# Kernel optimization log

Hardware: AMD Instinct MI355X
Metric: run time of the kernel (lower is better)

The kernel has to match this reference:

```python
import jax, jax.numpy as jnp
import numpy as np

B, F, H, K, E = 512, 1280, 2560, 8, 9  # batch, feat_dim, 2*feat_dim, branching, n_internal
# Tree: root=node 0 (expert 0); level-1 nodes 1..8 (experts 1..8); level-2 leaves 9..72.

def setup_inputs() -> dict:
    key = jax.random.key(0)
    k0, k1, k2, k3, k4 = jax.random.split(key, 5)
    x = jax.random.normal(k0, (B, F), dtype=jnp.float32)
    W1 = jax.random.normal(k1, (E, F, H), dtype=jnp.float32) / np.sqrt(F)
    b1 = jnp.zeros((E, H), dtype=jnp.float32)
    W2 = jax.random.normal(k2, (E, H, K), dtype=jnp.float32) / np.sqrt(H)
    b2 = jnp.zeros((E, K), dtype=jnp.float32)
    return {"x": x, "W1": W1, "b1": b1, "W2": W2, "b2": b2}

def reference(x, W1, b1, W2, b2):
    # Batched experts: Linear(F->H) -> ReLU -> Linear(H->K), softmax over children.
    h = jax.nn.relu(jnp.einsum('bf,efh->ebh', x, W1) + b1[:, None, :])  # [E,B,H]
    logits = jnp.einsum('ebh,ehk->ebk', h, W2) + b2[:, None, :]          # [E,B,K]
    probs = jax.nn.softmax(logits, axis=-1)                              # [E,B,K]
    # Path products root->node for every node (matches leaf_probs in torch code).
    p0 = jnp.ones((1, x.shape[0]), dtype=x.dtype)        # root: prob 1        [1,B]
    p1 = probs[0].T                                       # nodes 1..8          [K,B]
    # leaves 9..72: parent of node n is 1+(n-9)//K, child index (n-9)%K
    p2 = (p1[:, None, :] * jnp.transpose(probs[1:E], (0, 2, 1))).reshape(K * K, -1)  # [64,B]
    leaf_probs = jnp.concatenate([p0, p1, p2], axis=0).T  # [B, 73]
    return leaf_probs, logits
```

## Files before the change

### kernel.cpp

```cpp
#include <hip/hip_runtime.h>

#define TB 512
#define TF 1280
#define TH 2560
#define TK 8
#define TE 9

typedef __attribute__((ext_vector_type(8))) short short8;
typedef __attribute__((ext_vector_type(4))) short short4v;
typedef __attribute__((ext_vector_type(4))) float floatx4;

__device__ __forceinline__ short f2bf(float f) {
  union { float f; unsigned u; } v; v.f = f;
  unsigned r = v.u + 0x7fffu + ((v.u >> 16) & 1u);
  return (short)(r >> 16);
}

__global__ __launch_bounds__(256) void gemm1_relu(
    const float* __restrict__ x, const float* __restrict__ W1,
    const float* __restrict__ b1, short* __restrict__ h) {
  __shared__ __align__(16) short As[128 * 40];
  __shared__ __align__(16) short Bs[128 * 40];
  const int t = threadIdx.x;
  const int tileN = blockIdx.x;
  const int tileM = blockIdx.y;
  const int e = tileN / 20;
  const int hbase = (tileN % 20) * 128;
  const int m0 = tileM * 128;

  const int lane = t & 63, w = t >> 6;
  const int wm = w & 1, wn = w >> 1;
  const int lm = lane & 15, lq = lane >> 4;
  const int lk = lq * 8;

  floatx4 acc[4][4];
#pragma unroll
  for (int i = 0; i < 4; ++i)
#pragma unroll
    for (int j = 0; j < 4; ++j) acc[i][j] = (floatx4){0.f, 0.f, 0.f, 0.f};

  const float* wp = W1 + (long)e * TF * TH + hbase;
  const int cA = (t & 7) * 4;
  const int mA = t >> 3;
  const int nB = t & 127;
  const int gB = t >> 7;

  for (int kt = 0; kt < TF / 32; ++kt) {
    const int k0 = kt * 32;
    if (kt) __syncthreads();
#pragma unroll
    for (int i = 0; i < 4; ++i) {
      const int m = mA + 32 * i;
      floatx4 v = *(const floatx4*)(x + (long)(m0 + m) * TF + k0 + cA);
      short4v s; s.x = f2bf(v.x); s.y = f2bf(v.y); s.z = f2bf(v.z); s.w = f2bf(v.w);
      *(short4v*)&As[m * 40 + cA] = s;
    }
    {
      const float* bp = wp + (long)k0 * TH + nB;
#pragma unroll
      for (int q = 0; q < 4; ++q) {
        const int k4 = gB * 16 + q * 4;
        float f0 = bp[(long)(k4 + 0) * TH];
        float f1 = bp[(long)(k4 + 1) * TH];
        float f2 = bp[(long)(k4 + 2) * TH];
        float f3 = bp[(long)(k4 + 3) * TH];
        short4v s; s.x = f2bf(f0); s.y = f2bf(f1); s.z = f2bf(f2); s.w = f2bf(f3);
        *(short4v*)&Bs[nB * 40 + k4] = s;
      }
    }
    __syncthreads();
    short8 af[4], bfr[4];
#pragma unroll
    for (int mg = 0; mg < 4; ++mg)
      af[mg] = *(const short8*)&As[(wm * 64 + mg * 16 + lm) * 40 + lk];
#pragma unroll
    for (int ng = 0; ng < 4; ++ng)
      bfr[ng] = *(const short8*)&Bs[(wn * 64 + ng * 16 + lm) * 40 + lk];
#pragma unroll
    for (int mg = 0; mg < 4; ++mg)
#pragma unroll
      for (int ng = 0; ng < 4; ++ng)
        acc[mg][ng] = __builtin_amdgcn_mfma_f32_16x16x32_bf16(af[mg], bfr[ng], acc[mg][ng], 0, 0, 0);
  }

#pragma unroll
  for (int mg = 0; mg < 4; ++mg) {
    const int row = m0 + wm * 64 + mg * 16 + lq * 4;
#pragma unroll
    for (int ng = 0; ng < 4; ++ng) {
      const int col = hbase + wn * 64 + ng * 16 + lm;
      const float bias = b1[e * TH + col];
      floatx4 c = acc[mg][ng];
#pragma unroll
      for (int r = 0; r < 4; ++r) {
        float v = c[r] + bias;
        v = v > 0.f ? v : 0.f;
        h[((long)e * TB + row + r) * TH + col] = f2bf(v);
      }
    }
  }
}

__global__ __launch_bounds__(256) void gemm2_softmax(
    const short* __restrict__ h, const float* __restrict__ W2,
    const float* __restrict__ b2, float* __restrict__ logits_out,
    float* __restrict__ probs) {
  __shared__ __align__(16) short W2t[8 * 2568];
  const int t = threadIdx.x;
  const int e = blockIdx.x >> 3;
  const int bt = blockIdx.x & 7;

  {
    const int n = t & 7;
    const int kstart = (t >> 3) * 80;
    const float* wp = W2 + (long)e * TH * TK + n;
    for (int j = 0; j < 80; ++j) {
      const int k = kstart + j;
      W2t[n * 2568 + k] = f2bf(wp[(long)k * TK]);
    }
  }
  __syncthreads();

  const int lane = t & 63, w = t >> 6;
  const int lm = lane & 15, lq = lane >> 4, lk = lq * 8;
  const int rb = bt * 64 + w * 16;
  const short* hp = h + ((long)e * TB + rb + lm) * TH + lk;

  floatx4 acc = (floatx4){0.f, 0.f, 0.f, 0.f};
  const short8 zero8 = {0, 0, 0, 0, 0, 0, 0, 0};
  for (int kt = 0; kt < TH / 32; ++kt) {
    short8 a = *(const short8*)(hp + kt * 32);
    short8 b = (lm < 8) ? *(const short8*)&W2t[lm * 2568 + kt * 32 + lk] : zero8;
    acc = __builtin_amdgcn_mfma_f32_16x16x32_bf16(a, b, acc, 0, 0, 0);
  }

  const float bias = b2[e * TK + (lm & 7)];
  float lg[4], pr[4];
#pragma unroll
  for (int r = 0; r < 4; ++r) {
    float v = acc[r] + bias;
    float mx = v;
    mx = fmaxf(mx, __shfl_xor(mx, 1, 64));
    mx = fmaxf(mx, __shfl_xor(mx, 2, 64));
    mx = fmaxf(mx, __shfl_xor(mx, 4, 64));
    float ex = __expf(v - mx);
    float sm = ex;
    sm += __shfl_xor(sm, 1, 64);
    sm += __shfl_xor(sm, 2, 64);
    sm += __shfl_xor(sm, 4, 64);
    lg[r] = v;
    pr[r] = ex / sm;
  }
  if (lm < 8) {
#pragma unroll
    for (int r = 0; r < 4; ++r) {
      const long idx = ((long)e * TB + rb + lq * 4 + r) * TK + lm;
      logits_out[idx] = lg[r];
      probs[idx] = pr[r];
    }
  }
}

__global__ __launch_bounds__(256) void leafk(const float* __restrict__ probs,
                                             float* __restrict__ out) {
  const int idx = blockIdx.x * 256 + threadIdx.x;
  if (idx >= TB * 73) return;
  const int b = idx / 73, c = idx % 73;
  float v;
  if (c == 0) {
    v = 1.0f;
  } else if (c < 9) {
    v = probs[(long)b * TK + (c - 1)];
  } else {
    const int i = (c - 9) >> 3, j = (c - 9) & 7;
    v = probs[(long)b * TK + i] * probs[((long)(1 + i) * TB + b) * TK + j];
  }
  out[idx] = v;
}

extern "C" void kernel_launch(void* const* d_in, const int* in_sizes, int n_in,
                              void* d_out, int out_size, void* d_ws, size_t ws_size,
                              hipStream_t stream) {
  const float* x  = (const float*)d_in[0];
  const float* W1 = (const float*)d_in[1];
  const float* b1 = (const float*)d_in[2];
  const float* W2 = (const float*)d_in[3];
  const float* b2 = (const float*)d_in[4];
  float* out = (float*)d_out;

  short* h = (short*)d_ws;
  float* probs = (float*)((char*)d_ws + (size_t)TE * TB * TH * 2);
  float* logits_out = out + TB * 73;

  gemm1_relu<<<dim3(180, 4), 256, 0, stream>>>(x, W1, b1, h);
  gemm2_softmax<<<TE * 8, 256, 0, stream>>>(h, W2, b2, logits_out, probs);
  leafk<<<(TB * 73 + 255) / 256, 256, 0, stream>>>(probs, out);
}
```

Baseline: 241.5 us.

## Prepass bf16 conversion, async LDS loads, register-prefetched W1, split-K gemm2

Adds a prepass kernel that converts x to bf16 and transposes and converts W2 to bf16. gemm1 now loads A tiles straight into a swizzled LDS layout with global_load_lds and uses a K tile of 64. W1 loads are vectorised and prefetched into registers one step ahead. gemm2 splits K across four waves with an LDS reduction and runs on 4x more blocks. This targets the per-tile conversion cost, strided W1 loads and gemm2's low parallelism, at the cost of an extra launch and more register pressure.

After: 245.2 us. Within noise of the previous version (+1.5%).

```diff
diff --git a/kernel.cpp b/kernel.cpp
--- a/kernel.cpp
+++ b/kernel.cpp
@@ -6,32 +6,66 @@
 #define TK 8
 #define TE 9
 
+typedef unsigned short ushortT;
 typedef __attribute__((ext_vector_type(8))) short short8;
-typedef __attribute__((ext_vector_type(4))) short short4v;
 typedef __attribute__((ext_vector_type(4))) float floatx4;
 
-__device__ __forceinline__ short f2bf(float f) {
+__device__ __forceinline__ unsigned short f2bf(float f) {
   union { float f; unsigned u; } v; v.f = f;
   unsigned r = v.u + 0x7fffu + ((v.u >> 16) & 1u);
-  return (short)(r >> 16);
-}
-
-__global__ __launch_bounds__(256) void gemm1_relu(
-    const float* __restrict__ x, const float* __restrict__ W1,
-    const float* __restrict__ b1, short* __restrict__ h) {
-  __shared__ __align__(16) short As[128 * 40];
-  __shared__ __align__(16) short Bs[128 * 40];
+  return (unsigned short)(r >> 16);
+}
+
+__device__ __forceinline__ unsigned pk2(float a, float b) {
+  union { float f; unsigned u; } ua, ub; ua.f = a; ub.f = b;
+  unsigned ra = ua.u + 0x7fffu + ((ua.u >> 16) & 1u);
+  unsigned rb = ub.u + 0x7fffu + ((ub.u >> 16) & 1u);
+  return __builtin_amdgcn_perm(rb, ra, 0x07060302);
+}
+
+__device__ __forceinline__ void gl_lds16(const void* g, void* l) {
+  __builtin_amdgcn_global_load_lds(
+      (const __attribute__((address_space(1))) unsigned*)g,
+      (__attribute__((address_space(3))) unsigned*)l, 16, 0, 0);
+}
+
+__global__ __launch_bounds__(256) void prepass(
+    const float* __restrict__ x, const float* __restrict__ W2,
+    ushortT* __restrict__ xb, ushortT* __restrict__ W2t) {
+  const int i = blockIdx.x * 256 + threadIdx.x;
+  if (i < TB * TF / 2) {
+    float2 v = ((const float2*)x)[i];
+    ((unsigned*)xb)[i] = pk2(v.x, v.y);
+  } else {
+    const int o = i - TB * TF / 2;
+    if (o < TE * TK * TH) {
+      const int hcol = o % TH;
+      const int rest = o / TH;
+      const int n = rest & 7;
+      const int e = rest >> 3;
+      W2t[(long)(e * TK + n) * TH + hcol] = f2bf(W2[((long)e * TH + hcol) * TK + n]);
+    }
+  }
+}
+
+__global__ __launch_bounds__(256, 3) void gemm1_relu(
+    const ushortT* __restrict__ xb, const float* __restrict__ W1,
+    const float* __restrict__ b1, ushortT* __restrict__ h) {
+  __shared__ __align__(16) ushortT As[128 * 64];
+  __shared__ __align__(16) ushortT Bs[128 * 72];
+
   const int t = threadIdx.x;
   const int tileN = blockIdx.x;
-  const int tileM = blockIdx.y;
   const int e = tileN / 20;
   const int hbase = (tileN % 20) * 128;
-  const int m0 = tileM * 128;
+  const int m0 = blockIdx.y * 128;
 
   const int lane = t & 63, w = t >> 6;
   const int wm = w & 1, wn = w >> 1;
   const int lm = lane & 15, lq = lane >> 4;
-  const int lk = lq * 8;
+
+  const int kk4 = (t & 15) * 4;
+  const int n0 = (t >> 4) * 8;
 
   floatx4 acc[4][4];
 #pragma unroll
@@ -39,48 +73,65 @@
 #pragma unroll
     for (int j = 0; j < 4; ++j) acc[i][j] = (floatx4){0.f, 0.f, 0.f, 0.f};
 
-  const float* wp = W1 + (long)e * TF * TH + hbase;
-  const int cA = (t & 7) * 4;
-  const int mA = t >> 3;
-  const int nB = t & 127;
-  const int gB = t >> 7;
-
-  for (int kt = 0; kt < TF / 32; ++kt) {
-    const int k0 = kt * 32;
+  const float* wbase = W1 + ((long)e * TF) * TH + hbase + n0;
+
+  floatx4 bv[4][2];
+#pragma unroll
+  for (int r = 0; r < 4; ++r)
+#pragma unroll
+    for (int c = 0; c < 2; ++c)
+      bv[r][c] = *(const floatx4*)(wbase + (long)(kk4 + r) * TH + c * 4);
+
+  for (int kt = 0; kt < TF / 64; ++kt) {
+    const int k0 = kt * 64;
     if (kt) __syncthreads();
-#pragma unroll
-    for (int i = 0; i < 4; ++i) {
-      const int m = mA + 32 * i;
-      floatx4 v = *(const floatx4*)(x + (long)(m0 + m) * TF + k0 + cA);
-      short4v s; s.x = f2bf(v.x); s.y = f2bf(v.y); s.z = f2bf(v.z); s.w = f2bf(v.w);
-      *(short4v*)&As[m * 40 + cA] = s;
-    }
-    {
-      const float* bp = wp + (long)k0 * TH + nB;
-#pragma unroll
-      for (int q = 0; q < 4; ++q) {
-        const int k4 = gB * 16 + q * 4;
-        float f0 = bp[(long)(k4 + 0) * TH];
-        float f1 = bp[(long)(k4 + 1) * TH];
-        float f2 = bp[(long)(k4 + 2) * TH];
-        float f3 = bp[(long)(k4 + 3) * TH];
-        short4v s; s.x = f2bf(f0); s.y = f2bf(f1); s.z = f2bf(f2); s.w = f2bf(f3);
-        *(short4v*)&Bs[nB * 40 + k4] = s;
+
+#pragma unroll
+    for (int j = 0; j < 4; ++j) {
+      const int s = j * 256 + w * 64 + lane;
+      const int m = s >> 3;
+      const int cc = (s & 7) ^ (m & 7);
+      const ushortT* src = xb + (long)(m0 + m) * TF + k0 + cc * 8;
+      gl_lds16(src, (void*)&As[(j * 256 + w * 64) * 8]);
+    }
+#pragma unroll
+    for (int j = 0; j < 8; ++j) {
+      const int c = j >> 2, q = j & 3;
+      unsigned w0 = pk2(bv[0][c][q], bv[1][c][q]);
+      unsigned w1 = pk2(bv[2][c][q], bv[3][c][q]);
+      unsigned long long p = (unsigned long long)w0 | ((unsigned long long)w1 << 32);
+      *(unsigned long long*)&Bs[(n0 + j) * 72 + kk4] = p;
+    }
+    __syncthreads();
+
+    if (kt + 1 < TF / 64) {
+#pragma unroll
+      for (int r = 0; r < 4; ++r)
+#pragma unroll
+        for (int c = 0; c < 2; ++c)
+          bv[r][c] = *(const floatx4*)(wbase + (long)(k0 + 64 + kk4 + r) * TH + c * 4);
+    }
+
+#pragma unroll
+    for (int kk = 0; kk < 2; ++kk) {
+      short8 af[4], bf[4];
+#pragma unroll
+      for (int mg = 0; mg < 4; ++mg) {
+        const int m = wm * 64 + mg * 16 + lm;
+        const int swz = (kk * 4 + lq) ^ (m & 7);
+        af[mg] = *(const short8*)&As[m * 64 + swz * 8];
       }
-    }
-    __syncthreads();
-    short8 af[4], bfr[4];
-#pragma unroll
-    for (int mg = 0; mg < 4; ++mg)
-      af[mg] = *(const short8*)&As[(wm * 64 + mg * 16 + lm) * 40 + lk];
-#pragma unroll
-    for (int ng = 0; ng < 4; ++ng)
-      bfr[ng] = *(const short8*)&Bs[(wn * 64 + ng * 16 + lm) * 40 + lk];
-#pragma unroll
-    for (int mg = 0; mg < 4; ++mg)
-#pragma unroll
-      for (int ng = 0; ng < 4; ++ng)
-        acc[mg][ng] = __builtin_amdgcn_mfma_f32_16x16x32_bf16(af[mg], bfr[ng], acc[mg][ng], 0, 0, 0);
+#pragma unroll
+      for (int ng = 0; ng < 4; ++ng) {
+        const int n = wn * 64 + ng * 16 + lm;
+        bf[ng] = *(const short8*)&Bs[n * 72 + kk * 32 + lq * 8];
+      }
+#pragma unroll
+      for (int mg = 0; mg < 4; ++mg)
+#pragma unroll
+        for (int ng = 0; ng < 4; ++ng)
+          acc[mg][ng] = __builtin_amdgcn_mfma_f32_16x16x32_bf16(af[mg], bf[ng], acc[mg][ng], 0, 0, 0);
+    }
   }
 
 #pragma unroll
@@ -102,61 +153,50 @@
 }
 
 __global__ __launch_bounds__(256) void gemm2_softmax(
-    const short* __restrict__ h, const float* __restrict__ W2,
+    const ushortT* __restrict__ h, const ushortT* __restrict__ W2t,
     const float* __restrict__ b2, float* __restrict__ logits_out,
     float* __restrict__ probs) {
-  __shared__ __align__(16) short W2t[8 * 2568];
+  __shared__ float Ls[4][16][8];
   const int t = threadIdx.x;
-  const int e = blockIdx.x >> 3;
-  const int bt = blockIdx.x & 7;
-
-  {
-    const int n = t & 7;
-    const int kstart = (t >> 3) * 80;
-    const float* wp = W2 + (long)e * TH * TK + n;
-    for (int j = 0; j < 80; ++j) {
-      const int k = kstart + j;
-      W2t[n * 2568 + k] = f2bf(wp[(long)k * TK]);
-    }
+  const int lane = t & 63, w = t >> 6;
+  const int e = blockIdx.x >> 5;
+  const int r0 = (blockIdx.x & 31) * 16;
+  const int lm = lane & 15, lq = lane >> 4;
+
+  const ushortT* hp = h + ((long)(e * TB + r0 + lm)) * TH + w * 640 + lq * 8;
+  const int bn = lm < 8 ? lm : 7;
+  const ushortT* wp = W2t + ((long)(e * TK + bn)) * TH + w * 640 + lq * 8;
+
+  floatx4 acc = (floatx4){0.f, 0.f, 0.f, 0.f};
+#pragma unroll
+  for (int kt = 0; kt < 20; ++kt) {
+    short8 a = *(const short8*)(hp + kt * 32);
+    short8 b = *(const short8*)(wp + kt * 32);
+    acc = __builtin_amdgcn_mfma_f32_16x16x32_bf16(a, b, acc, 0, 0, 0);
+  }
+  if (lm < 8) {
+#pragma unroll
+    for (int r = 0; r < 4; ++r) Ls[w][lq * 4 + r][lm] = acc[r];
   }
   __syncthreads();
-
-  const int lane = t & 63, w = t >> 6;
-  const int lm = lane & 15, lq = lane >> 4, lk = lq * 8;
-  const int rb = bt * 64 + w * 16;
-  const short* hp = h + ((long)e * TB + rb + lm) * TH + lk;
-
-  floatx4 acc = (floatx4){0.f, 0.f, 0.f, 0.f};
-  const short8 zero8 = {0, 0, 0, 0, 0, 0, 0, 0};
-  for (int kt = 0; kt < TH / 32; ++kt) {
-    short8 a = *(const short8*)(hp + kt * 32);
-    short8 b = (lm < 8) ? *(const short8*)&W2t[lm * 2568 + kt * 32 + lk] : zero8;
-    acc = __builtin_amdgcn_mfma_f32_16x16x32_bf16(a, b, acc, 0, 0, 0);
-  }
-
-  const float bias = b2[e * TK + (lm & 7)];
-  float lg[4], pr[4];
-#pragma unroll
-  for (int r = 0; r < 4; ++r) {
-    float v = acc[r] + bias;
-    float mx = v;
-    mx = fmaxf(mx, __shfl_xor(mx, 1, 64));
-    mx = fmaxf(mx, __shfl_xor(mx, 2, 64));
-    mx = fmaxf(mx, __shfl_xor(mx, 4, 64));
-    float ex = __expf(v - mx);
-    float sm = ex;
-    sm += __shfl_xor(sm, 1, 64);
-    sm += __shfl_xor(sm, 2, 64);
-    sm += __shfl_xor(sm, 4, 64);
-    lg[r] = v;
-    pr[r] = ex / sm;
-  }
-  if (lm < 8) {
+  if (w == 0 && lm < 8) {
+    const float bias = b2[e * TK + lm];
 #pragma unroll
     for (int r = 0; r < 4; ++r) {
-      const long idx = ((long)e * TB + rb + lq * 4 + r) * TK + lm;
-      logits_out[idx] = lg[r];
-      probs[idx] = pr[r];
+      const int row = lq * 4 + r;
+      float v = Ls[0][row][lm] + Ls[1][row][lm] + Ls[2][row][lm] + Ls[3][row][lm] + bias;
+      float mx = v;
+      mx = fmaxf(mx, __shfl_xor(mx, 1, 64));
+      mx = fmaxf(mx, __shfl_xor(mx, 2, 64));
+      mx = fmaxf(mx, __shfl_xor(mx, 4, 64));
+      float ex = __expf(v - mx);
+      float sm = ex;
+      sm += __shfl_xor(sm, 1, 64);
+      sm += __shfl_xor(sm, 2, 64);
+      sm += __shfl_xor(sm, 4, 64);
+      const long idx = ((long)e * TB + r0 + row) * TK + lm;
+      logits_out[idx] = v;
+      probs[idx] = ex / sm;
     }
   }
 }
@@ -188,11 +228,14 @@
   const float* b2 = (const float*)d_in[4];
   float* out = (float*)d_out;
 
-  short* h = (short*)d_ws;
-  float* probs = (float*)((char*)d_ws + (size_t)TE * TB * TH * 2);
+  ushortT* h      = (ushortT*)d_ws;
+  float*   probs  = (float*)((char*)d_ws + 23592960);
+  ushortT* xb     = (ushortT*)((char*)d_ws + 23740416);
+  ushortT* W2t    = (ushortT*)((char*)d_ws + 25051136);
   float* logits_out = out + TB * 73;
 
-  gemm1_relu<<<dim3(180, 4), 256, 0, stream>>>(x, W1, b1, h);
-  gemm2_softmax<<<TE * 8, 256, 0, stream>>>(h, W2, b2, logits_out, probs);
+  prepass<<<2000, 256, 0, stream>>>(x, W2, xb, W2t);
+  gemm1_relu<<<dim3(180, 4), 256, 0, stream>>>(xb, W1, b1, h);
+  gemm2_softmax<<<TE * 32, 256, 0, stream>>>(h, W2t, b2, logits_out, probs);
   leafk<<<(TB * 73 + 255) / 256, 256, 0, stream>>>(probs, out);
 }
```
